# Kernel optimization log

Hardware: AMD Instinct MI355X
Metric: run time of the kernel (lower is better)

## Reference

```python
import jax, jax.numpy as jnp
import numpy as np

B, L, D, H = 2, 2048, 1024, 16
C = D // H  # head dim = 64
SCALE = 1.0 / np.sqrt(D).astype(np.float32)  # note: 1/sqrt(in_c), full dim, per source


def setup_inputs() -> dict:
    key = jax.random.key(0)
    ks = jax.random.split(key, 5)
    return {
        "x": jax.random.normal(ks[0], (B, L, D), dtype=jnp.float32),
        "w_qkv": jax.random.normal(ks[1], (3 * D, D), dtype=jnp.float32) * (1.0 / np.sqrt(D)),
        "b_qkv": jax.random.normal(ks[2], (3 * D,), dtype=jnp.float32) * 0.02,
        "w_o": jax.random.normal(ks[3], (D, D), dtype=jnp.float32) * (1.0 / np.sqrt(D)),
        "b_o": jax.random.normal(ks[4], (D,), dtype=jnp.float32) * 0.02,
    }


def reference(x, w_qkv, b_qkv, w_o, b_o):
    b, l, d = x.shape
    h, c = H, d // H
    # fused QKV projection: torch Linear is x @ W.T + b
    qkv = jnp.einsum('bld,ed->ble', x, w_qkv) + b_qkv  # [B, L, 3D]
    q, k, v = jnp.split(qkv, 3, axis=-1)
    q = q.reshape(b, l, h, c)
    k = k.reshape(b, l, h, c)
    v = v.reshape(b, l, h, c)
    # attention scores [B, H, L, L], scaled by 1/sqrt(in_c)
    attn = jax.nn.softmax(jnp.einsum('blhc,bmhc->bhlm', q, k) * SCALE, axis=-1)
    heads = jnp.einsum('bhlm,bmhc->blhc', attn, v).reshape(b, l, d)
    return jnp.einsum('bld,ed->ble', heads, w_o) + b_o + x
```

## Files before the change

kernel.cpp:

```cpp
#include <hip/hip_runtime.h>
#include <hip/hip_bf16.h>
#include <stdint.h>

typedef _Float16 half_t;
typedef _Float16 half4 __attribute__((ext_vector_type(4)));
typedef _Float16 half8 __attribute__((ext_vector_type(8)));
typedef float f32x4 __attribute__((ext_vector_type(4)));

#define SCALE2_ 0.045084220f

#if __has_builtin(__builtin_amdgcn_exp2f)
#define EXP2F(x) __builtin_amdgcn_exp2f(x)
#else
#define EXP2F(x) exp2f(x)
#endif

#define GLL16(g, l)                                                        \
  __builtin_amdgcn_global_load_lds(                                        \
      (const __attribute__((address_space(1))) void*)(g),                  \
      (__attribute__((address_space(3))) void*)(l), 16, 0, 0)

#define WAITVM(N) asm volatile("s_waitcnt vmcnt(" #N ")" ::: "memory")
#define BAR() __builtin_amdgcn_s_barrier()
#define SCHEDB() __builtin_amdgcn_sched_barrier(0)

__global__ void cvt_all(const float* __restrict__ x,
                        const float* __restrict__ wqkv,
                        const float* __restrict__ wo,
                        half_t* __restrict__ xb,
                        half_t* __restrict__ wqkvb,
                        half_t* __restrict__ wob) {
  int i = blockIdx.x * blockDim.x + threadIdx.x;
  const float* src; half_t* dst; int off;
  if (i < 1048576)       { src = x;    dst = xb;    off = i; }
  else if (i < 1835008)  { src = wqkv; dst = wqkvb; off = i - 1048576; }
  else                   { src = wo;   dst = wob;   off = i - 1835008; }
  float4 v = ((const float4*)src)[off];
  half4 h;
  h[0] = (half_t)v.x; h[1] = (half_t)v.y; h[2] = (half_t)v.z; h[3] = (half_t)v.w;
  ((half4*)dst)[off] = h;
}

__global__ __launch_bounds__(256) void qkv_gemm(
    const half_t* __restrict__ A, const half_t* __restrict__ Bw,
    const float* __restrict__ bias,
    half_t* __restrict__ Qh, half_t* __restrict__ Kh, half_t* __restrict__ Vt) {
  __shared__ __align__(16) half_t As[2][128 * 32];
  __shared__ __align__(16) half_t Bs[2][128 * 32];
  const int tid = threadIdx.x;
  const int wave = tid >> 6, lane = tid & 63;
  const int t = lane & 15, g = lane >> 4;
  const int wr = (wave >> 1) * 64, wc = (wave & 1) * 64;
  const int hw = blockIdx.x;
  const int swzid = (hw & 7) * 96 + (hw >> 3);
  const int m0 = (swzid / 24) * 128, n0 = (swzid % 24) * 128;

  f32x4 acc[4][4];
#pragma unroll
  for (int i = 0; i < 4; ++i)
#pragma unroll
    for (int j = 0; j < 4; ++j) acc[i][j] = (f32x4){0.f, 0.f, 0.f, 0.f};

  const int r0 = tid >> 2;
  const int colb = ((tid & 3) * 16) ^ ((r0 & 3) << 4);
  const half_t* aptr = A + (size_t)(m0 + r0) * 1024 + (colb >> 1);
  const half_t* bptr = Bw + (size_t)(n0 + r0) * 1024 + (colb >> 1);
  const int swz = (t & 3) << 4;

#define QSTG(b, kkt)                                                          \
  {                                                                           \
    _Pragma("unroll")                                                         \
    for (int is = 0; is < 2; ++is) {                                          \
      GLL16(aptr + (size_t)(kkt) * 32 + (size_t)is * 64 * 1024,               \
            (char*)As + (b) * 8192 + wave * 1024 + is * 4096);                \
      GLL16(bptr + (size_t)(kkt) * 32 + (size_t)is * 64 * 1024,               \
            (char*)Bs + (b) * 8192 + wave * 1024 + is * 4096);                \
    }                                                                         \
  }

  QSTG(0, 0);
  for (int kk = 0; kk < 32; ++kk) {
    QSTG((kk + 1) & 1, (kk + 1) & 31);
    WAITVM(4);
    BAR(); SCHEDB();
    const char* as = (const char*)As + (kk & 1) * 8192;
    const char* bs = (const char*)Bs + (kk & 1) * 8192;
    half8 af[4], bf[4];
#pragma unroll
    for (int fm = 0; fm < 4; ++fm)
      af[fm] = *(const half8*)(as + (wr + fm * 16 + t) * 64 + ((g * 16) ^ swz));
#pragma unroll
    for (int fn = 0; fn < 4; ++fn)
      bf[fn] = *(const half8*)(bs + (wc + fn * 16 + t) * 64 + ((g * 16) ^ swz));
#pragma unroll
    for (int fm = 0; fm < 4; ++fm)
#pragma unroll
      for (int fn = 0; fn < 4; ++fn)
        acc[fm][fn] = __builtin_amdgcn_mfma_f32_16x16x32_f16(
            af[fm], bf[fn], acc[fm][fn], 0, 0, 0);
    BAR();
  }
#undef QSTG

#pragma unroll
  for (int fm = 0; fm < 4; ++fm) {
    const int mb = m0 + wr + fm * 16 + g * 4;
#pragma unroll
    for (int fn = 0; fn < 4; ++fn) {
      const int n = n0 + wc + fn * 16 + t;
      const float bv = bias[n];
      const int sec = n >> 10, nn = n & 1023;
      const int h = nn >> 6, c = nn & 63;
#pragma unroll
      for (int r = 0; r < 4; ++r) {
        const int mm = mb + r;
        const int b = mm >> 11, l = mm & 2047;
        const float v = acc[fm][fn][r] + bv;
        const size_t bh = (size_t)(b * 16 + h);
        if (sec == 0)      Qh[(bh * 2048 + l) * 64 + c] = (half_t)(v * SCALE2_);
        else if (sec == 1) Kh[(bh * 2048 + l) * 64 + c] = (half_t)v;
        else {
          const int lp = (l & ~63) |
                         (((l >> 2) & 3) * 16 + ((l >> 4) & 3) * 4 + (l & 3));
          Vt[(bh * 64 + c) * 2048 + lp] = (half_t)v;
        }
      }
    }
  }
}

__global__ __launch_bounds__(512) void attn_kernel(
    const half_t* __restrict__ Qh, const half_t* __restrict__ Kh,
    const half_t* __restrict__ Vt, half_t* __restrict__ Hd) {
  __shared__ __align__(16) char lds_raw[2][2][8192];
  const int hw = blockIdx.x;
  const int swzid = (hw & 7) * 64 + (hw >> 3);
  const int bh = swzid >> 4;
  const int qt = swzid & 15;
  const int tid = threadIdx.x;
  const int wave = tid >> 6, lane = tid & 63;
  const int t = lane & 15, g = lane >> 4;

  const half_t* Q = Qh + ((size_t)bh * 2048 + qt * 128 + wave * 16) * 64;
  const half8 q0 = *(const half8*)&Q[t * 64 + g * 8];
  const half8 q1 = *(const half8*)&Q[t * 64 + 32 + g * 8];

  const int r0 = tid >> 3;
  const int colb = ((tid & 7) * 16) ^ ((r0 & 7) << 4);
  const half_t* kbase = Kh + (size_t)bh * 2048 * 64 + (size_t)r0 * 64 + (colb >> 1);
  const half_t* vbase = Vt + (size_t)bh * 64 * 2048 + (size_t)r0 * 2048 + (colb >> 1);

  const int swz = (t & 7) << 4;
  const int vk0 = t * 128 + ((g * 16) ^ swz);
  const int vk1 = t * 128 + ((64 + g * 16) ^ swz);
  const int vv0 = t * 128 + ((g * 32) ^ swz);
  const int vv1 = t * 128 + ((g * 32 + 16) ^ swz);

  f32x4 o[4];
#pragma unroll
  for (int i = 0; i < 4; ++i) o[i] = (f32x4){0.f, 0.f, 0.f, 0.f};
  float lsum = 0.f;
  const f32x4 cinit = (f32x4){-8.f, -8.f, -8.f, -8.f};

#define STG(b, tt)                                                     \
  {                                                                    \
    GLL16(kbase + (size_t)(tt) * 4096, (char*)lds_raw[b][0] + wave * 1024); \
    GLL16(vbase + (size_t)(tt) * 64,   (char*)lds_raw[b][1] + wave * 1024); \
  }

  STG(0, 0);
  for (int it = 0; it < 32; ++it) {
    STG((it + 1) & 1, (it + 1) & 31);
    WAITVM(2);
    BAR(); SCHEDB();

    const char* kb = lds_raw[it & 1][0];
    const char* vb = lds_raw[it & 1][1];

    f32x4 s4[4];
    __builtin_amdgcn_s_setprio(1);
#pragma unroll
    for (int st = 0; st < 4; ++st) {
      half8 k0 = *(const half8*)(kb + vk0 + st * 2048);
      half8 k1 = *(const half8*)(kb + vk1 + st * 2048);
      f32x4 a = __builtin_amdgcn_mfma_f32_16x16x32_f16(k0, q0, cinit, 0, 0, 0);
      a = __builtin_amdgcn_mfma_f32_16x16x32_f16(k1, q1, a, 0, 0, 0);
      s4[st] = a;
    }
    __builtin_amdgcn_s_setprio(0);

    half4 pf[4];
#pragma unroll
    for (int st = 0; st < 4; ++st) {
      const float p0 = EXP2F(s4[st][0]);
      const float p1 = EXP2F(s4[st][1]);
      const float p2 = EXP2F(s4[st][2]);
      const float p3 = EXP2F(s4[st][3]);
      lsum += (p0 + p1) + (p2 + p3);
      pf[st][0] = (half_t)p0; pf[st][1] = (half_t)p1;
      pf[st][2] = (half_t)p2; pf[st][3] = (half_t)p3;
    }

    __builtin_amdgcn_s_setprio(1);
#pragma unroll
    for (int sthalf = 0; sthalf < 2; ++sthalf) {
      const int voff = sthalf ? vv1 : vv0;
#pragma unroll
      for (int ct = 0; ct < 4; ++ct) {
        half8 vv = *(const half8*)(vb + voff + ct * 2048);
        half4 vlo = {vv[0], vv[1], vv[2], vv[3]};
        half4 vhi = {vv[4], vv[5], vv[6], vv[7]};
        o[ct] = __builtin_amdgcn_mfma_f32_16x16x16f16(pf[2 * sthalf], vlo,
                                                      o[ct], 0, 0, 0);
        o[ct] = __builtin_amdgcn_mfma_f32_16x16x16f16(pf[2 * sthalf + 1], vhi,
                                                      o[ct], 0, 0, 0);
      }
    }
    __builtin_amdgcn_s_setprio(0);

    BAR();
  }
#undef STG

  lsum += __shfl_xor(lsum, 16);
  lsum += __shfl_xor(lsum, 32);

  const int b = bh >> 4, h = bh & 15;
#pragma unroll
  for (int r = 0; r < 4; ++r) {
    const float li = 1.f / __shfl(lsum, (g << 2) + r);
    const size_t row = (size_t)b * 2048 + qt * 128 + wave * 16 + g * 4 + r;
#pragma unroll
    for (int ct = 0; ct < 4; ++ct)
      Hd[row * 1024 + h * 64 + ct * 16 + t] = (half_t)(o[ct][r] * li);
  }
}

__global__ __launch_bounds__(256) void out_gemm(
    const half_t* __restrict__ A, const half_t* __restrict__ Bw,
    const float* __restrict__ bias, const float* __restrict__ xres,
    float* __restrict__ out) {
  __shared__ __align__(16) half_t As[2][64 * 32];
  __shared__ __align__(16) half_t Bs[2][128 * 32];
  const int tid = threadIdx.x;
  const int wave = tid >> 6, lane = tid & 63;
  const int t = lane & 15, g = lane >> 4;
  const int wr = (wave >> 1) * 32, wc = (wave & 1) * 64;
  const int hw = blockIdx.x;
  const int swzid = (hw & 7) * 64 + (hw >> 3);
  const int m0 = (swzid >> 3) * 64, n0 = (swzid & 7) * 128;

  f32x4 acc[2][4];
#pragma unroll
  for (int i = 0; i < 2; ++i)
#pragma unroll
    for (int j = 0; j < 4; ++j) acc[i][j] = (f32x4){0.f, 0.f, 0.f, 0.f};

  const int r0 = tid >> 2;
  const int colb = ((tid & 3) * 16) ^ ((r0 & 3) << 4);
  const half_t* aptr = A + (size_t)(m0 + r0) * 1024 + (colb >> 1);
  const half_t* bptr = Bw + (size_t)(n0 + r0) * 1024 + (colb >> 1);
  const int swz = (t & 3) << 4;

#define OSTG(b, kkt)                                                          \
  {                                                                           \
    GLL16(aptr + (size_t)(kkt) * 32,                                          \
          (char*)As + (b) * 4096 + wave * 1024);                              \
    _Pragma("unroll")                                                         \
    for (int is = 0; is < 2; ++is)                                            \
      GLL16(bptr + (size_t)(kkt) * 32 + (size_t)is * 64 * 1024,               \
            (char*)Bs + (b) * 8192 + wave * 1024 + is * 4096);                \
  }

  OSTG(0, 0);
  for (int kk = 0; kk < 32; ++kk) {
    OSTG((kk + 1) & 1, (kk + 1) & 31);
    WAITVM(3);
    BAR(); SCHEDB();
    const char* as = (const char*)As + (kk & 1) * 4096;
    const char* bs = (const char*)Bs + (kk & 1) * 8192;
    half8 af[2], bf[4];
#pragma unroll
    for (int fm = 0; fm < 2; ++fm)
      af[fm] = *(const half8*)(as + (wr + fm * 16 + t) * 64 + ((g * 16) ^ swz));
#pragma unroll
    for (int fn = 0; fn < 4; ++fn)
      bf[fn] = *(const half8*)(bs + (wc + fn * 16 + t) * 64 + ((g * 16) ^ swz));
#pragma unroll
    for (int fm = 0; fm < 2; ++fm)
#pragma unroll
      for (int fn = 0; fn < 4; ++fn)
        acc[fm][fn] = __builtin_amdgcn_mfma_f32_16x16x32_f16(
            af[fm], bf[fn], acc[fm][fn], 0, 0, 0);
    BAR();
  }
#undef OSTG

#pragma unroll
  for (int fm = 0; fm < 2; ++fm) {
    const int mb = m0 + wr + fm * 16 + g * 4;
#pragma unroll
    for (int fn = 0; fn < 4; ++fn) {
      const int n = n0 + wc + fn * 16 + t;
      const float bv = bias[n];
#pragma unroll
      for (int r = 0; r < 4; ++r) {
        const size_t idx = (size_t)(mb + r) * 1024 + n;
        out[idx] = acc[fm][fn][r] + bv + xres[idx];
      }
    }
  }
}

extern "C" void kernel_launch(void* const* d_in, const int* in_sizes, int n_in,
                              void* d_out, int out_size, void* d_ws, size_t ws_size,
                              hipStream_t stream) {
  const float* x     = (const float*)d_in[0];
  const float* w_qkv = (const float*)d_in[1];
  const float* b_qkv = (const float*)d_in[2];
  const float* w_o   = (const float*)d_in[3];
  const float* b_o   = (const float*)d_in[4];
  float* out = (float*)d_out;

  char* ws = (char*)d_ws;
  half_t* xb    = (half_t*)(ws + 0);
  half_t* wqkvb = (half_t*)(ws + (size_t)8  * 1048576);
  half_t* wob   = (half_t*)(ws + (size_t)14 * 1048576);
  half_t* Qh    = (half_t*)(ws + (size_t)16 * 1048576);
  half_t* Kh    = (half_t*)(ws + (size_t)24 * 1048576);
  half_t* Vt    = (half_t*)(ws + (size_t)32 * 1048576);
  half_t* Hd    = (half_t*)(ws + (size_t)40 * 1048576);

  cvt_all<<<8192, 256, 0, stream>>>(x, w_qkv, w_o, xb, wqkvb, wob);
  qkv_gemm<<<768, 256, 0, stream>>>(xb, wqkvb, b_qkv, Qh, Kh, Vt);
  attn_kernel<<<512, 512, 0, stream>>>(Qh, Kh, Vt, Hd);
  out_gemm<<<512, 256, 0, stream>>>(Hd, wob, b_o, x, out);
}
```

Baseline: 211.8 us.

## Triple-buffer LDS staging in QKV GEMM, attention and output GEMM

Each of the three kernels now uses three LDS buffers instead of two and prefetches two tiles ahead, with the vmcnt wait relaxed to match. This gives global-to-LDS loads more time to land before they are consumed, which should hide memory latency better. The cost is 50% more shared memory per block, which can lower occupancy, and redundant reloads of the last tile at the end of the loop.

Result: slower. 216.7 us (+2.3%).

```diff
diff --git a/kernel.cpp b/kernel.cpp
--- a/kernel.cpp
+++ b/kernel.cpp
@@ -45,8 +45,8 @@
     const half_t* __restrict__ A, const half_t* __restrict__ Bw,
     const float* __restrict__ bias,
     half_t* __restrict__ Qh, half_t* __restrict__ Kh, half_t* __restrict__ Vt) {
-  __shared__ __align__(16) half_t As[2][128 * 32];
-  __shared__ __align__(16) half_t Bs[2][128 * 32];
+  __shared__ __align__(16) half_t As[3][128 * 32];
+  __shared__ __align__(16) half_t Bs[3][128 * 32];
   const int tid = threadIdx.x;
   const int wave = tid >> 6, lane = tid & 63;
   const int t = lane & 15, g = lane >> 4;
@@ -79,12 +79,16 @@
   }
 
   QSTG(0, 0);
+  QSTG(1, 1);
+  int cur = 0;
   for (int kk = 0; kk < 32; ++kk) {
-    QSTG((kk + 1) & 1, (kk + 1) & 31);
-    WAITVM(4);
+    int kt = kk + 2; if (kt > 31) kt = 31;
+    int sl = cur + 2; if (sl >= 3) sl -= 3;
+    QSTG(sl, kt);
+    WAITVM(8);
     BAR(); SCHEDB();
-    const char* as = (const char*)As + (kk & 1) * 8192;
-    const char* bs = (const char*)Bs + (kk & 1) * 8192;
+    const char* as = (const char*)As + cur * 8192;
+    const char* bs = (const char*)Bs + cur * 8192;
     half8 af[4], bf[4];
 #pragma unroll
     for (int fm = 0; fm < 4; ++fm)
@@ -99,6 +103,7 @@
         acc[fm][fn] = __builtin_amdgcn_mfma_f32_16x16x32_f16(
             af[fm], bf[fn], acc[fm][fn], 0, 0, 0);
     BAR();
+    cur = cur + 1; if (cur >= 3) cur = 0;
   }
 #undef QSTG
 
@@ -132,7 +137,7 @@
 __global__ __launch_bounds__(512) void attn_kernel(
     const half_t* __restrict__ Qh, const half_t* __restrict__ Kh,
     const half_t* __restrict__ Vt, half_t* __restrict__ Hd) {
-  __shared__ __align__(16) char lds_raw[2][2][8192];
+  __shared__ __align__(16) char lds_raw[3][2][8192];
   const int hw = blockIdx.x;
   const int swzid = (hw & 7) * 64 + (hw >> 3);
   const int bh = swzid >> 4;
@@ -169,13 +174,17 @@
   }
 
   STG(0, 0);
+  STG(1, 1);
+  int cur = 0;
   for (int it = 0; it < 32; ++it) {
-    STG((it + 1) & 1, (it + 1) & 31);
-    WAITVM(2);
+    int tt = it + 2; if (tt > 31) tt = 31;
+    int sl = cur + 2; if (sl >= 3) sl -= 3;
+    STG(sl, tt);
+    WAITVM(4);
     BAR(); SCHEDB();
 
-    const char* kb = lds_raw[it & 1][0];
-    const char* vb = lds_raw[it & 1][1];
+    const char* kb = lds_raw[cur][0];
+    const char* vb = lds_raw[cur][1];
 
     f32x4 s4[4];
     __builtin_amdgcn_s_setprio(1);
@@ -219,6 +228,7 @@
     __builtin_amdgcn_s_setprio(0);
 
     BAR();
+    cur = cur + 1; if (cur >= 3) cur = 0;
   }
 #undef STG
 
@@ -240,8 +250,8 @@
     const half_t* __restrict__ A, const half_t* __restrict__ Bw,
     const float* __restrict__ bias, const float* __restrict__ xres,
     float* __restrict__ out) {
-  __shared__ __align__(16) half_t As[2][64 * 32];
-  __shared__ __align__(16) half_t Bs[2][128 * 32];
+  __shared__ __align__(16) half_t As[3][64 * 32];
+  __shared__ __align__(16) half_t Bs[3][128 * 32];
   const int tid = threadIdx.x;
   const int wave = tid >> 6, lane = tid & 63;
   const int t = lane & 15, g = lane >> 4;
@@ -273,12 +283,16 @@
   }
 
   OSTG(0, 0);
+  OSTG(1, 1);
+  int cur = 0;
   for (int kk = 0; kk < 32; ++kk) {
-    OSTG((kk + 1) & 1, (kk + 1) & 31);
-    WAITVM(3);
+    int kt = kk + 2; if (kt > 31) kt = 31;
+    int sl = cur + 2; if (sl >= 3) sl -= 3;
+    OSTG(sl, kt);
+    WAITVM(6);
     BAR(); SCHEDB();
-    const char* as = (const char*)As + (kk & 1) * 4096;
-    const char* bs = (const char*)Bs + (kk & 1) * 8192;
+    const char* as = (const char*)As + cur * 4096;
+    const char* bs = (const char*)Bs + cur * 8192;
     half8 af[2], bf[4];
 #pragma unroll
     for (int fm = 0; fm < 2; ++fm)
@@ -293,6 +307,7 @@
         acc[fm][fn] = __builtin_amdgcn_mfma_f32_16x16x32_f16(
             af[fm], bf[fn], acc[fm][fn], 0, 0, 0);
     BAR();
+    cur = cur + 1; if (cur >= 3) cur = 0;
   }
 #undef OSTG
 
```
